# Kernel optimization log

Measured on AMD Instinct MI355X. Metric: run time of the kernel, lower is better.

## Reference

```python
import jax, jax.numpy as jnp
import numpy as np
import itertools

F = 20        # field_size
D = 16        # embedding_size / output_dims
H = 2         # num_hash
NB = 500000   # num_buckets
B = 4096      # batch
NI = F * (F - 1) // 2  # 190 pairwise interactions


def _interact_indexes(field_size):
    # For each field i, indices of the C(F,2) combinations that contain i -> [F, F-1]
    combos = list(itertools.combinations(range(field_size), 2))
    idx = [[j for j, c in enumerate(combos) if i in c] for i in range(field_size)]
    return np.asarray(idx, dtype=np.int32)


def setup_inputs() -> dict:
    key = jax.random.key(0)
    k0, k1, k2, k3, k4, k5 = jax.random.split(key, 6)
    return {
        "origin_embeddings": jax.random.normal(k0, (B, F, D), jnp.float32),
        "codebook": jax.random.normal(k1, (NB, D), jnp.float32) * 0.01,
        "W_transform": jax.random.normal(k2, (H * D, D), jnp.float32) * 0.05,
        "senet_w1": jax.random.normal(k3, (F * D, F * D), jnp.float32) * 0.02,
        "senet_w2": jax.random.normal(k4, (F * D, NI), jnp.float32) * 0.02,
        # Precomputed hash bucket ids (stands in for the StrongHash of string tokens)
        "hash_idx": jax.random.randint(k5, (H, B, NI), 0, NB, dtype=jnp.int32),
        "interact_indexes": jnp.asarray(_interact_indexes(F)),
    }


def reference(origin_embeddings, codebook, W_transform, senet_w1, senet_w2, hash_idx, interact_indexes):
    b = origin_embeddings.shape[0]
    # multi-hash codebook gathers (hash-share: one codebook): [H, B, NI, D]
    gathered = codebook[hash_idx]
    # merge_mode='concat' over hash functions -> [B, NI, H*D]
    emb = jnp.concatenate([gathered[i] for i in range(gathered.shape[0])], axis=-1)
    # hash_merge_final_transform: Dense(output_dims, no bias) -> [B, NI, D]
    emb = jnp.einsum('bne,ed->bnd', emb, W_transform)
    # SENET (bit squeeze, ratio 1.0, vector excitation, no activation) over origin embeddings
    z = origin_embeddings.reshape(b, -1)          # [B, F*D]
    w = (z @ senet_w1) @ senet_w2                 # [B, NI]
    # gather each field's interactions and weighted-sum ('senetsum')
    field_emb = emb[:, interact_indexes]          # [B, F, F-1, D]
    field_w = w[:, interact_indexes][..., None]   # [B, F, F-1, 1]
    out = jnp.sum(field_emb * field_w, axis=-2)   # [B, F, D]
    return out
```

## Files before the change

kernel.cpp:

```cpp
#include <hip/hip_runtime.h>

#define FF 20
#define DD 16
#define EE 32
#define NI 190
#define BB 4096
#define FD 320

__global__ __launch_bounds__(192) void k_w12(const float* __restrict__ w1,
                                             const float* __restrict__ w2,
                                             float* __restrict__ W12) {
    __shared__ float srow[FD];
    int r = blockIdx.x;
    for (int j = threadIdx.x; j < FD; j += 192) srow[j] = w1[r * FD + j];
    __syncthreads();
    int c = threadIdx.x;
    if (c < NI) {
        float acc = 0.f;
        for (int k = 0; k < FD; ++k) acc += srow[k] * w2[k * NI + c];
        W12[r * NI + c] = acc;
    }
}

__global__ __launch_bounds__(192) void k_w(const float* __restrict__ z,
                                           const float* __restrict__ W12,
                                           float* __restrict__ wout) {
    __shared__ float sz[8 * FD];
    int b0 = blockIdx.x * 8;
    for (int j = threadIdx.x; j < 8 * FD; j += 192) sz[j] = z[b0 * FD + j];
    __syncthreads();
    int c = threadIdx.x;
    if (c < NI) {
        float acc[8] = {0.f, 0.f, 0.f, 0.f, 0.f, 0.f, 0.f, 0.f};
        for (int k = 0; k < FD; ++k) {
            float wv = W12[k * NI + c];
#pragma unroll
            for (int bb = 0; bb < 8; ++bb) acc[bb] += sz[bb * FD + k] * wv;
        }
#pragma unroll
        for (int bb = 0; bb < 8; ++bb) wout[(b0 + bb) * NI + c] = acc[bb];
    }
}

__global__ __launch_bounds__(256) void k_main(const float* __restrict__ cb,
                                              const float* __restrict__ Wt,
                                              const int* __restrict__ hidx,
                                              const int* __restrict__ iidx,
                                              const float* __restrict__ wbuf,
                                              float* __restrict__ out) {
    __shared__ float s_rows[32 * 32];
    __shared__ float s_embw[NI * 16];
    __shared__ int s_i0[NI], s_i1[NI];
    __shared__ float s_w[NI];
    __shared__ int s_pii[FF * (FF - 1)];

    int t = threadIdx.x;
    int b = blockIdx.x;

    for (int j = t; j < NI; j += 256) {
        s_i0[j] = hidx[b * NI + j];
        s_i1[j] = hidx[BB * NI + b * NI + j];
        s_w[j] = wbuf[b * NI + j];
    }
    for (int j = t; j < FF * (FF - 1); j += 256) s_pii[j] = iidx[j];

    int d = t & 15;
    float Wr[32];
#pragma unroll
    for (int k = 0; k < 32; ++k) Wr[k] = Wt[k * 16 + d];
    __syncthreads();

    const float4* cb4 = (const float4*)cb;
    int pp_st = t >> 3;
    int q = t & 7;
    int h = q >> 2;
    int cq = q & 3;
    int pgrp = t >> 4;

    for (int base = 0; base < NI; base += 32) {
        int pair = base + pp_st;
        if (pair < NI) {
            int row = h ? s_i1[pair] : s_i0[pair];
            float4 v = cb4[row * 4 + cq];
            *(float4*)&s_rows[pp_st * 32 + h * 16 + cq * 4] = v;
        }
        __syncthreads();
#pragma unroll
        for (int pg = 0; pg < 2; ++pg) {
            int pp = pgrp + pg * 16;
            int pair2 = base + pp;
            if (pair2 < NI) {
                const float* r = &s_rows[pp * 32];
                float acc = 0.f;
#pragma unroll
                for (int k = 0; k < 32; ++k) acc += r[k] * Wr[k];
                s_embw[pair2 * 16 + d] = acc * s_w[pair2];
            }
        }
        __syncthreads();
    }

    for (int o = t; o < FD; o += 256) {
        int i = o >> 4;
        int dd = o & 15;
        float acc = 0.f;
#pragma unroll
        for (int s = 0; s < FF - 1; ++s) {
            int j = s_pii[i * (FF - 1) + s];
            acc += s_embw[j * 16 + dd];
        }
        out[b * FD + o] = acc;
    }
}

extern "C" void kernel_launch(void* const* d_in, const int* in_sizes, int n_in,
                              void* d_out, int out_size, void* d_ws, size_t ws_size,
                              hipStream_t stream) {
    const float* origin = (const float*)d_in[0];
    const float* cb     = (const float*)d_in[1];
    const float* Wt     = (const float*)d_in[2];
    const float* w1     = (const float*)d_in[3];
    const float* w2     = (const float*)d_in[4];
    const int*   hidx   = (const int*)d_in[5];
    const int*   iidx   = (const int*)d_in[6];
    float* out = (float*)d_out;

    float* W12  = (float*)d_ws;
    float* wbuf = W12 + FD * NI;

    k_w12<<<FD, 192, 0, stream>>>(w1, w2, W12);
    k_w<<<BB / 8, 192, 0, stream>>>(origin, W12, wbuf);
    k_main<<<BB, 256, 0, stream>>>(cb, Wt, hidx, iidx, wbuf, out);
}
```

Measured before the change: 154.2 us.

## Gather all codebook rows up front in k_main and pad shared-memory strides

k_main now issues every codebook gather for all 190 pairs in one pass into a larger padded shared buffer, followed by a single barrier. This replaces the 6-round gather/compute loop that had two barriers per round, so more global loads are in flight at once. Row and embedding strides are padded (36 and 17) to reduce LDS bank conflicts, and the dot product reads float4. k_w also processes 16 batch rows per block instead of 8, raising reuse of W12. The cost is roughly 40KB of LDS per block, which may lower occupancy.

```diff
diff --git a/kernel.cpp b/kernel.cpp
--- a/kernel.cpp
+++ b/kernel.cpp
@@ -2,10 +2,11 @@
 
 #define FF 20
 #define DD 16
-#define EE 32
 #define NI 190
 #define BB 4096
 #define FD 320
+#define RSTR 36
+#define ESTR 17
 
 __global__ __launch_bounds__(192) void k_w12(const float* __restrict__ w1,
                                              const float* __restrict__ w2,
@@ -25,20 +26,22 @@
 __global__ __launch_bounds__(192) void k_w(const float* __restrict__ z,
                                            const float* __restrict__ W12,
                                            float* __restrict__ wout) {
-    __shared__ float sz[8 * FD];
-    int b0 = blockIdx.x * 8;
-    for (int j = threadIdx.x; j < 8 * FD; j += 192) sz[j] = z[b0 * FD + j];
+    __shared__ float sz[16 * FD];
+    int b0 = blockIdx.x * 16;
+    for (int j = threadIdx.x; j < 16 * FD; j += 192) sz[j] = z[b0 * FD + j];
     __syncthreads();
     int c = threadIdx.x;
     if (c < NI) {
-        float acc[8] = {0.f, 0.f, 0.f, 0.f, 0.f, 0.f, 0.f, 0.f};
+        float acc[16];
+#pragma unroll
+        for (int bb = 0; bb < 16; ++bb) acc[bb] = 0.f;
         for (int k = 0; k < FD; ++k) {
             float wv = W12[k * NI + c];
 #pragma unroll
-            for (int bb = 0; bb < 8; ++bb) acc[bb] += sz[bb * FD + k] * wv;
+            for (int bb = 0; bb < 16; ++bb) acc[bb] += sz[bb * FD + k] * wv;
         }
 #pragma unroll
-        for (int bb = 0; bb < 8; ++bb) wout[(b0 + bb) * NI + c] = acc[bb];
+        for (int bb = 0; bb < 16; ++bb) wout[(b0 + bb) * NI + c] = acc[bb];
     }
 }
 
@@ -48,8 +51,8 @@
                                               const int* __restrict__ iidx,
                                               const float* __restrict__ wbuf,
                                               float* __restrict__ out) {
-    __shared__ float s_rows[32 * 32];
-    __shared__ float s_embw[NI * 16];
+    __shared__ float s_rows[NI * RSTR];
+    __shared__ float s_embw[NI * ESTR];
     __shared__ int s_i0[NI], s_i1[NI];
     __shared__ float s_w[NI];
     __shared__ int s_pii[FF * (FF - 1)];
@@ -71,34 +74,35 @@
     __syncthreads();
 
     const float4* cb4 = (const float4*)cb;
-    int pp_st = t >> 3;
-    int q = t & 7;
-    int h = q >> 2;
-    int cq = q & 3;
-    int pgrp = t >> 4;
+    for (int tt = t; tt < NI * 8; tt += 256) {
+        int pair = tt >> 3;
+        int half = (tt >> 2) & 1;
+        int chunk = tt & 3;
+        int row = half ? s_i1[pair] : s_i0[pair];
+        float4 v = cb4[row * 4 + chunk];
+        *(float4*)&s_rows[pair * RSTR + half * 16 + chunk * 4] = v;
+    }
+    __syncthreads();
 
-    for (int base = 0; base < NI; base += 32) {
-        int pair = base + pp_st;
+    int pp = t >> 4;
+#pragma unroll
+    for (int rnd = 0; rnd < 12; ++rnd) {
+        int pair = rnd * 16 + pp;
         if (pair < NI) {
-            int row = h ? s_i1[pair] : s_i0[pair];
-            float4 v = cb4[row * 4 + cq];
-            *(float4*)&s_rows[pp_st * 32 + h * 16 + cq * 4] = v;
+            const float4* r4 = (const float4*)&s_rows[pair * RSTR];
+            float acc = 0.f;
+#pragma unroll
+            for (int c = 0; c < 8; ++c) {
+                float4 v = r4[c];
+                acc += v.x * Wr[c * 4 + 0];
+                acc += v.y * Wr[c * 4 + 1];
+                acc += v.z * Wr[c * 4 + 2];
+                acc += v.w * Wr[c * 4 + 3];
+            }
+            s_embw[pair * ESTR + d] = acc * s_w[pair];
         }
-        __syncthreads();
-#pragma unroll
-        for (int pg = 0; pg < 2; ++pg) {
-            int pp = pgrp + pg * 16;
-            int pair2 = base + pp;
-            if (pair2 < NI) {
-                const float* r = &s_rows[pp * 32];
-                float acc = 0.f;
-#pragma unroll
-                for (int k = 0; k < 32; ++k) acc += r[k] * Wr[k];
-                s_embw[pair2 * 16 + d] = acc * s_w[pair2];
-            }
-        }
-        __syncthreads();
     }
+    __syncthreads();
 
     for (int o = t; o < FD; o += 256) {
         int i = o >> 4;
@@ -107,7 +111,7 @@
 #pragma unroll
         for (int s = 0; s < FF - 1; ++s) {
             int j = s_pii[i * (FF - 1) + s];
-            acc += s_embw[j * 16 + dd];
+            acc += s_embw[j * ESTR + dd];
         }
         out[b * FD + o] = acc;
     }
@@ -129,6 +133,6 @@
     float* wbuf = W12 + FD * NI;
 
     k_w12<<<FD, 192, 0, stream>>>(w1, w2, W12);
-    k_w<<<BB / 8, 192, 0, stream>>>(origin, W12, wbuf);
+    k_w<<<BB / 16, 192, 0, stream>>>(origin, W12, wbuf);
     k_main<<<BB, 256, 0, stream>>>(cb, Wt, hidx, iidx, wbuf, out);
 }
```

Result: slower. 170.4 us (+10.5%).
